# Performance work log

Measured on AMD Instinct MI355X. Metric: run time of the kernel, lower is better.

## Reference

```python
import jax, jax.numpy as jnp
import numpy as np

# FusionTransformer with input_resolution=(1, 8192): window_size collapses to 1,
# shift_size forced to 0, attn_mask is None. Inside WindowAttention each window
# has N=1 token, so the 512-truncation and the stride-2 subsample are no-ops,
# softmax over a single key yields 1, and the attention output equals v.
# We still compute q/k, the scaled logit, the relative-position bias (index
# table is [[0]]) and the softmax faithfully.

B, L, C = 8, 8192, 384
NH, CS = 8, 3
DIN = C // CS              # 128 = dim // channel_scale
HD = C // NH // CS         # 16  = per-head qk/v dim
SCALE = (C // NH) ** -0.5  # uses head_dim = dim // num_heads = 48 (as in source)
HID = int(DIN * 4.0)       # 512 mlp hidden
EPS = 1e-5                 # torch LayerNorm default


def setup_inputs() -> dict:
    key = jax.random.key(0)
    ks = jax.random.split(key, 8)
    w = lambda k, shape: jax.random.normal(k, shape, jnp.float32) * 0.02
    return {
        "x": jax.random.normal(ks[0], (B, L, C), jnp.float32),
        "g1": jnp.ones((C,), jnp.float32), "b1": jnp.zeros((C,), jnp.float32),
        "Wq": w(ks[1], (C, DIN)), "bq": jnp.zeros((DIN,), jnp.float32),
        "Wkv": w(ks[2], (C, 2 * DIN)), "bkv": jnp.zeros((2 * DIN,), jnp.float32),
        "rpb": w(ks[3], (1, NH)),  # (2*ws-1)^2 = 1 table rows at ws=1
        "Wp": w(ks[4], (DIN, DIN)), "bp": jnp.zeros((DIN,), jnp.float32),
        "g2": jnp.ones((DIN,), jnp.float32), "b2": jnp.zeros((DIN,), jnp.float32),
        "W1": w(ks[5], (DIN, HID)), "bm1": jnp.zeros((HID,), jnp.float32),
        "W2": w(ks[6], (HID, DIN)), "bm2": jnp.zeros((DIN,), jnp.float32),
    }


def _ln(x, g, b):
    m = x.mean(-1, keepdims=True)
    v = ((x - m) ** 2).mean(-1, keepdims=True)
    return (x - m) * jax.lax.rsqrt(v + EPS) * g + b


def reference(x, g1, b1, Wq, bq, Wkv, bkv, rpb, Wp, bp, g2, b2, W1, bm1, W2, bm2):
    Bx, Lx, _ = x.shape
    h = _ln(x, g1, b1)                       # norm1
    # window partition with ws=1: every token is a (N=1) window; B_ = B*L.
    q = h @ Wq + bq                          # (B, L, DIN)
    kv = h @ Wkv + bkv                       # (B, L, 2*DIN); split dim-0 of the
    k, v = kv[..., :DIN], kv[..., DIN:]      # reshape(...,2,NH,HD) -> k, v
    qh = q.reshape(Bx, Lx, NH, HD)
    kh = k.reshape(Bx, Lx, NH, HD)
    vh = v.reshape(Bx, Lx, NH, HD)
    # attn logits (B, L, NH, 1, 1) flattened: q*scale . k + rel-pos bias[idx=0]
    logits = jnp.einsum('blhd,blhd->blh', qh * SCALE, kh) + rpb[0]
    attn = jax.nn.softmax(logits[..., None], axis=-1)   # softmax over N=1 keys
    out = (attn * vh).reshape(Bx, Lx, NH * HD)          # attn @ v, heads merged
    y = out @ Wp + bp                                   # proj
    # residual branch: x = attn_out; x = x + mlp(norm2(x))
    z = y + (jax.nn.gelu(_ln(y, g2, b2) @ W1 + bm1, approximate=False) @ W2 + bm2)
    return z
```

## Files before the change

### kernel.cpp

```cpp
#include <hip/hip_runtime.h>
#include <hip/hip_bf16.h>
#include <stdint.h>


typedef __attribute__((ext_vector_type(8))) short bf16x8;
typedef __attribute__((ext_vector_type(4))) float f32x4;

__device__ __forceinline__ short f2bf(float f) {
  union { float f; unsigned u; } a; a.f = f;
  unsigned u = a.u;
  u += 0x7fffu + ((u >> 16) & 1u);
  return (short)(u >> 16);
}
__device__ __forceinline__ float bf2f(short s) {
  union { unsigned u; float f; } a; a.u = ((unsigned)(unsigned short)s) << 16;
  return a.f;
}
__device__ __forceinline__ float gelu_fast(float h) {
  float h2 = h * h;
  float w  = h * (2.3022082f + 0.1029471f * h2);
  float e  = __builtin_amdgcn_exp2f(w);
  float r  = __builtin_amdgcn_rcpf(e + 1.0f);
  return h - h * r;
}
__device__ __forceinline__ void gload_lds16(const void* g, void* l) {
  __builtin_amdgcn_global_load_lds(
      (const __attribute__((address_space(1))) unsigned*)g,
      (__attribute__((address_space(3))) unsigned*)l, 16, 0, 0);
}


__global__ void prep(const float* __restrict__ Wkv, const float* __restrict__ bkv,
                     const float* __restrict__ Wp,  const float* __restrict__ bp,
                     const float* __restrict__ W1,  const float* __restrict__ W2,
                     const float* __restrict__ g1,  const float* __restrict__ b1,
                     const float* __restrict__ g2,  const float* __restrict__ b2,
                     const float* __restrict__ bm1,
                     short* __restrict__ WcT, short* __restrict__ W1Ta,
                     short* __restrict__ W1Tb, short* __restrict__ W2Ta,
                     short* __restrict__ W2Tb, float* __restrict__ bc,
                     float* __restrict__ bm1c) {
  const int b = blockIdx.x, tid = threadIdx.x;
  if (b < 192) {
    __shared__ float wv[2][128];
    const int kk = tid >> 7, n = tid & 127, k = 2 * b + kk;
    wv[kk][n] = Wkv[k * 256 + 128 + n];
    __syncthreads();
    float s0 = 0, s1 = 0, s2 = 0, s3 = 0;
#pragma unroll 8
    for (int m = 0; m < 128; m += 4) {
      s0 += wv[kk][m]     * Wp[(m)     * 128 + n];
      s1 += wv[kk][m + 1] * Wp[(m + 1) * 128 + n];
      s2 += wv[kk][m + 2] * Wp[(m + 2) * 128 + n];
      s3 += wv[kk][m + 3] * Wp[(m + 3) * 128 + n];
    }
    WcT[n * 392 + k] = f2bf(g1[k] * (s0 + s1 + s2 + s3));
  } else if (b == 192) {
    __shared__ float t[128];
    if (tid < 128) {
      float a0 = 0, a1 = 0, a2 = 0, a3 = 0;
#pragma unroll 8
      for (int k = 0; k < 384; k += 4) {
        a0 += b1[k]     * Wkv[(k)     * 256 + 128 + tid];
        a1 += b1[k + 1] * Wkv[(k + 1) * 256 + 128 + tid];
        a2 += b1[k + 2] * Wkv[(k + 2) * 256 + 128 + tid];
        a3 += b1[k + 3] * Wkv[(k + 3) * 256 + 128 + tid];
      }
      t[tid] = a0 + a1 + a2 + a3 + bkv[128 + tid];
    }
    __syncthreads();
    if (tid < 128) {
      float s = bp[tid];
#pragma unroll 8
      for (int m = 0; m < 128; ++m) s += t[m] * Wp[m * 128 + tid];
      bc[tid] = s;
    }
  } else if (b < 449) {
    const int id = (b - 193) * 256 + tid;
    const int n = id & 511, k = id >> 9;
    const short v = f2bf(W1[k * 512 + n] * g2[k]);
    if (n < 256) W1Ta[n * 132 + k] = v;
    else         W1Tb[(n - 256) * 132 + k] = v;
  } else if (b < 705) {
    const int id = (b - 449) * 256 + tid;
    const int n = id & 127, k = id >> 7;
    const int ch = k >> 6, kk = k & 63;
    short* dst = (ch < 4) ? W2Ta : W2Tb;
    dst[((ch & 3) * 128 + n) * 68 + kk] = f2bf(W2[k * 128 + n]);
  } else {
    const int h = (b - 705) * 256 + tid;
    float s = bm1[h];
#pragma unroll 8
    for (int k = 0; k < 128; ++k) s += b2[k] * W1[k * 512 + h];
    bm1c[h] = s;
  }
}

__global__ __launch_bounds__(1024)
void k1(const float* __restrict__ x, const short* __restrict__ WcTg,
        const float* __restrict__ bcg,
        short* __restrict__ yb, short* __restrict__ lb) {
  __shared__ __align__(16) short WcT_l[128 * 392];
  __shared__ float bcf[128], css[128];
  const int tid = threadIdx.x, lane = tid & 63, w = tid >> 6;
  const int q = lane >> 4, c16 = lane & 15;

  for (int c = w; c < 98; c += 16)
    gload_lds16((const char*)WcTg + c * 1024 + lane * 16, (char*)WcT_l + c * 1024);
  if (tid < 32) ((float4*)bcf)[tid] = ((const float4*)bcg)[tid];
  __syncthreads();
  if (tid < 128) {
    float s0 = 0, s1 = 0, s2 = 0, s3 = 0;
    const short* row = WcT_l + tid * 392;
#pragma unroll 12
    for (int k = 0; k < 384; k += 4) {
      s0 += bf2f(row[k]); s1 += bf2f(row[k + 1]);
      s2 += bf2f(row[k + 2]); s3 += bf2f(row[k + 3]);
    }
    css[tid] = s0 + s1 + s2 + s3;
  }
  __syncthreads();

  const long band = (long)blockIdx.x * 16 + w;
  const float* xp = x + (band * 16 + c16) * 384 + q * 8;
  f32x4 yacc[8];
#pragma unroll
  for (int t = 0; t < 8; ++t) yacc[t] = (f32x4){0.f, 0.f, 0.f, 0.f};
  float s = 0.f, sq = 0.f;
#pragma unroll
  for (int ks = 0; ks < 12; ++ks) {
    const float4 va = *(const float4*)(xp + ks * 32);
    const float4 vb = *(const float4*)(xp + ks * 32 + 4);
    s  += va.x + va.y + va.z + va.w + vb.x + vb.y + vb.z + vb.w;
    sq += va.x * va.x + va.y * va.y + va.z * va.z + va.w * va.w
        + vb.x * vb.x + vb.y * vb.y + vb.z * vb.z + vb.w * vb.w;
    bf16x8 f;
    f[0] = f2bf(va.x); f[1] = f2bf(va.y); f[2] = f2bf(va.z); f[3] = f2bf(va.w);
    f[4] = f2bf(vb.x); f[5] = f2bf(vb.y); f[6] = f2bf(vb.z); f[7] = f2bf(vb.w);
#pragma unroll
    for (int t = 0; t < 8; ++t) {
      bf16x8 bfr = *(const bf16x8*)(WcT_l + (t * 16 + c16) * 392 + ks * 32 + q * 8);
      yacc[t] = __builtin_amdgcn_mfma_f32_16x16x32_bf16(f, bfr, yacc[t], 0, 0, 0);
    }
  }
  s  += __shfl_xor(s, 16);  s  += __shfl_xor(s, 32);
  sq += __shfl_xor(sq, 16); sq += __shfl_xor(sq, 32);
  const float mean = s * (1.f / 384.f);
  const float rs = rsqrtf(sq * (1.f / 384.f) - mean * mean + 1e-5f);
  float mr[4], rr[4];
#pragma unroll
  for (int r = 0; r < 4; ++r) {
    mr[r] = __shfl(mean, q * 4 + r);
    rr[r] = __shfl(rs,   q * 4 + r);
  }
  float sm[4] = {0, 0, 0, 0}, sv[4] = {0, 0, 0, 0};
#pragma unroll
  for (int t = 0; t < 8; ++t) {
    const float cst = css[t * 16 + c16];
    const float bct = bcf[t * 16 + c16];
#pragma unroll
    for (int r = 0; r < 4; ++r) {
      const float yv = rr[r] * (yacc[t][r] - mr[r] * cst) + bct;
      yacc[t][r] = yv; sm[r] += yv; sv[r] += yv * yv;
    }
  }
#pragma unroll
  for (int r = 0; r < 4; ++r) {
    sm[r] += __shfl_xor(sm[r], 1); sm[r] += __shfl_xor(sm[r], 2);
    sm[r] += __shfl_xor(sm[r], 4); sm[r] += __shfl_xor(sm[r], 8);
    sv[r] += __shfl_xor(sv[r], 1); sv[r] += __shfl_xor(sv[r], 2);
    sv[r] += __shfl_xor(sv[r], 4); sv[r] += __shfl_xor(sv[r], 8);
  }
  short* ybB = yb + band * 2048;
  short* lbB = lb + band * 2048;
#pragma unroll
  for (int r = 0; r < 4; ++r) {
    const float mn = sm[r] * (1.f / 128.f);
    const float rv = rsqrtf(sv[r] * (1.f / 128.f) - mn * mn + 1e-5f);
    bf16x8 yp;
#pragma unroll
    for (int t = 0; t < 8; ++t) {
      const float yv = yacc[t][r];
      yp[t] = f2bf(yv);
      lbB[((t * 4 + r) * 4 + q) * 16 + c16] = f2bf((yv - mn) * rv);
    }
    *(bf16x8*)(ybB + ((r * 4 + q) * 16 + c16) * 8) = yp;
  }
}

template <bool FINAL>
__global__ __launch_bounds__(1024)
void k2(const short* __restrict__ lb, short* __restrict__ ybuf,
        const short* __restrict__ W1Tg, const short* __restrict__ W2Tg,
        const float* __restrict__ bm1h, const float* __restrict__ bm2,
        float* __restrict__ out) {
  __shared__ __align__(16) short W1s[256 * 132];
  __shared__ __align__(16) short W2s[4 * 128 * 68];
  __shared__ __align__(16) short A3s[16][16 * 36];
  __shared__ float bm1s[256], bm2s[128];
  const int tid = threadIdx.x, lane = tid & 63, w = tid >> 6;
  const int q = lane >> 4, c16 = lane & 15;

  for (int c = w; c < 66; c += 16)
    gload_lds16((const char*)W1Tg + c * 1024 + lane * 16, (char*)W1s + c * 1024);
  for (int c = w; c < 68; c += 16)
    gload_lds16((const char*)W2Tg + c * 1024 + lane * 16, (char*)W2s + c * 1024);
  if (tid < 64) ((float4*)bm1s)[tid] = ((const float4*)bm1h)[tid];
  else if (tid < 96) ((float4*)bm2s)[tid - 64] = ((const float4*)bm2)[tid - 64];
  __syncthreads();

  const long band = (long)blockIdx.x * 16 + w;
  const short* lbB = lb + band * 2048;
  short* ybB = ybuf + band * 2048;
  bf16x8 a2f[4];
#pragma unroll
  for (int ks = 0; ks < 4; ++ks) {
    const int t = ks * 2 + (q >> 1);
    a2f[ks] = *(const bf16x8*)(lbB + ((t * 4 + (c16 & 3)) * 4 + (c16 >> 2)) * 16 + (q & 1) * 8);
  }
  f32x4 zacc[8];
#pragma unroll
  for (int t = 0; t < 8; ++t) zacc[t] = (f32x4){0.f, 0.f, 0.f, 0.f};
  short* a3 = A3s[w];

#pragma unroll
  for (int ch = 0; ch < 4; ++ch) {
#pragma unroll
    for (int sub = 0; sub < 2; ++sub) {
      f32x4 hacc[2];
      hacc[0] = (f32x4){0.f, 0.f, 0.f, 0.f};
      hacc[1] = (f32x4){0.f, 0.f, 0.f, 0.f};
#pragma unroll
      for (int ks = 0; ks < 4; ++ks)
#pragma unroll
        for (int tt = 0; tt < 2; ++tt) {
          bf16x8 bfr = *(const bf16x8*)(W1s + (ch * 64 + sub * 32 + tt * 16 + c16) * 132 + ks * 32 + q * 8);
          hacc[tt] = __builtin_amdgcn_mfma_f32_16x16x32_bf16(a2f[ks], bfr, hacc[tt], 0, 0, 0);
        }
#pragma unroll
      for (int tt = 0; tt < 2; ++tt) {
        const float bb = bm1s[ch * 64 + sub * 32 + tt * 16 + c16];
#pragma unroll
        for (int r = 0; r < 4; ++r) {
          const float h = hacc[tt][r] + bb;
          a3[(q * 4 + r) * 36 + tt * 16 + c16] = f2bf(gelu_fast(h));
        }
      }
      asm volatile("s_waitcnt lgkmcnt(0)" ::: "memory");
      bf16x8 af = *(const bf16x8*)(a3 + c16 * 36 + q * 8);
#pragma unroll
      for (int t = 0; t < 8; ++t) {
        bf16x8 bfr = *(const bf16x8*)(W2s + (ch * 128 + t * 16 + c16) * 68 + sub * 32 + q * 8);
        zacc[t] = __builtin_amdgcn_mfma_f32_16x16x32_bf16(af, bfr, zacc[t], 0, 0, 0);
      }
    }
  }
  bf16x8 yf[4];
#pragma unroll
  for (int r = 0; r < 4; ++r)
    yf[r] = *(const bf16x8*)(ybB + ((r * 4 + q) * 16 + c16) * 8);
  if (!FINAL) {
#pragma unroll
    for (int r = 0; r < 4; ++r) {
      bf16x8 zp;
#pragma unroll
      for (int t = 0; t < 8; ++t) zp[t] = f2bf(bf2f(yf[r][t]) + zacc[t][r]);
      *(bf16x8*)(ybB + ((r * 4 + q) * 16 + c16) * 8) = zp;
    }
  } else {
#pragma unroll
    for (int r = 0; r < 4; ++r) {
      const long rowg = band * 16 + q * 4 + r;
#pragma unroll
      for (int t = 0; t < 8; ++t)
        out[rowg * 128 + t * 16 + c16] = bf2f(yf[r][t]) + zacc[t][r] + bm2s[t * 16 + c16];
    }
  }
}

extern "C" void kernel_launch(void* const* d_in, const int* in_sizes, int n_in,
                              void* d_out, int out_size, void* d_ws, size_t ws_size,
                              hipStream_t stream) {
  const float* x   = (const float*)d_in[0];
  const float* g1  = (const float*)d_in[1];
  const float* b1  = (const float*)d_in[2];
  const float* Wkv = (const float*)d_in[5];
  const float* bkv = (const float*)d_in[6];
  const float* Wp  = (const float*)d_in[8];
  const float* bp  = (const float*)d_in[9];
  const float* g2  = (const float*)d_in[10];
  const float* b2  = (const float*)d_in[11];
  const float* W1  = (const float*)d_in[12];
  const float* bm1 = (const float*)d_in[13];
  const float* W2  = (const float*)d_in[14];
  const float* bm2 = (const float*)d_in[15];

  char* ws = (char*)d_ws;
  short* WcT  = (short*)(ws + 0);
  short* W1Ta = (short*)(ws + 100352);
  short* W2Ta = (short*)(ws + 167936);
  short* W1Tb = (short*)(ws + 237568);
  short* W2Tb = (short*)(ws + 305152);
  float* bc   = (float*)(ws + 374784);
  float* bm1c = (float*)(ws + 375296);
  short* ybuf = (short*)(ws + 378880);
  short* lb   = (short*)(ws + 17156096);

  prep<<<707, 256, 0, stream>>>(Wkv, bkv, Wp, bp, W1, W2, g1, b1, g2, b2, bm1,
                                WcT, W1Ta, W1Tb, W2Ta, W2Tb, bc, bm1c);
  k1<<<256, 1024, 0, stream>>>(x, WcT, bc, ybuf, lb);
  k2<false><<<256, 1024, 0, stream>>>(lb, ybuf, W1Ta, W2Ta, bm1c, bm2, (float*)d_out);
  k2<true><<<256, 1024, 0, stream>>>(lb, ybuf, W1Tb, W2Tb, bm1c + 256, bm2, (float*)d_out);
}
```

Before: 258.2 us.

## Fuse LN/projection and two MLP-half kernels into one kernel

Merges k1 and the two k2 launches into a single kernel. The kernel keeps y and the normalized activations in registers and reuses one shared-memory buffer, loading first the combined projection weights and then each MLP half's W1/W2 in turn. This removes the bf16 round trips through the ybuf/lb workspace and two kernel launches. In exchange, weight reloads now sit on each block's critical path behind barriers, and the large LDS footprint keeps occupancy at one block per CU.

New measurement: 335.5 us. 30.0% more time.

```diff
diff --git a/kernel.cpp b/kernel.cpp
--- a/kernel.cpp
+++ b/kernel.cpp
@@ -97,18 +97,25 @@
 }
 
 __global__ __launch_bounds__(1024)
-void k1(const float* __restrict__ x, const short* __restrict__ WcTg,
-        const float* __restrict__ bcg,
-        short* __restrict__ yb, short* __restrict__ lb) {
-  __shared__ __align__(16) short WcT_l[128 * 392];
-  __shared__ float bcf[128], css[128];
+void fused(const float* __restrict__ x, const short* __restrict__ WcTg,
+           const float* __restrict__ bcg,
+           const short* __restrict__ W1Tag, const short* __restrict__ W2Tag,
+           const short* __restrict__ W1Tbg, const short* __restrict__ W2Tbg,
+           const float* __restrict__ bm1c, const float* __restrict__ bm2,
+           float* __restrict__ out) {
+  __shared__ __align__(16) char Wbuf[137216];
+  __shared__ __align__(16) short A3s[16][576];
+  __shared__ float bcf[128], css[128], bm1s[512], bm2s[128];
   const int tid = threadIdx.x, lane = tid & 63, w = tid >> 6;
   const int q = lane >> 4, c16 = lane & 15;
 
   for (int c = w; c < 98; c += 16)
-    gload_lds16((const char*)WcTg + c * 1024 + lane * 16, (char*)WcT_l + c * 1024);
-  if (tid < 32) ((float4*)bcf)[tid] = ((const float4*)bcg)[tid];
+    gload_lds16((const char*)WcTg + c * 1024 + lane * 16, Wbuf + c * 1024);
+  if (tid < 128)      ((float4*)bm1s)[tid]       = ((const float4*)bm1c)[tid];
+  else if (tid < 160) ((float4*)bm2s)[tid - 128] = ((const float4*)bm2)[tid - 128];
+  else if (tid < 192) ((float4*)bcf)[tid - 160]  = ((const float4*)bcg)[tid - 160];
   __syncthreads();
+  const short* WcT_l = (const short*)Wbuf;
   if (tid < 128) {
     float s0 = 0, s1 = 0, s2 = 0, s3 = 0;
     const short* row = WcT_l + tid * 392;
@@ -153,6 +160,13 @@
     mr[r] = __shfl(mean, q * 4 + r);
     rr[r] = __shfl(rs,   q * 4 + r);
   }
+  __syncthreads();
+
+  for (int c = w; c < 66; c += 16)
+    gload_lds16((const char*)W1Tag + c * 1024 + lane * 16, Wbuf + c * 1024);
+  for (int c = w; c < 68; c += 16)
+    gload_lds16((const char*)W2Tag + c * 1024 + lane * 16, Wbuf + 67584 + c * 1024);
+
   float sm[4] = {0, 0, 0, 0}, sv[4] = {0, 0, 0, 0};
 #pragma unroll
   for (int t = 0; t < 8; ++t) {
@@ -171,110 +185,85 @@
     sv[r] += __shfl_xor(sv[r], 1); sv[r] += __shfl_xor(sv[r], 2);
     sv[r] += __shfl_xor(sv[r], 4); sv[r] += __shfl_xor(sv[r], 8);
   }
-  short* ybB = yb + band * 2048;
-  short* lbB = lb + band * 2048;
+  float mn[4], rv[4];
 #pragma unroll
   for (int r = 0; r < 4; ++r) {
-    const float mn = sm[r] * (1.f / 128.f);
-    const float rv = rsqrtf(sv[r] * (1.f / 128.f) - mn * mn + 1e-5f);
-    bf16x8 yp;
-#pragma unroll
-    for (int t = 0; t < 8; ++t) {
-      const float yv = yacc[t][r];
-      yp[t] = f2bf(yv);
-      lbB[((t * 4 + r) * 4 + q) * 16 + c16] = f2bf((yv - mn) * rv);
-    }
-    *(bf16x8*)(ybB + ((r * 4 + q) * 16 + c16) * 8) = yp;
-  }
-}
-
-template <bool FINAL>
-__global__ __launch_bounds__(1024)
-void k2(const short* __restrict__ lb, short* __restrict__ ybuf,
-        const short* __restrict__ W1Tg, const short* __restrict__ W2Tg,
-        const float* __restrict__ bm1h, const float* __restrict__ bm2,
-        float* __restrict__ out) {
-  __shared__ __align__(16) short W1s[256 * 132];
-  __shared__ __align__(16) short W2s[4 * 128 * 68];
-  __shared__ __align__(16) short A3s[16][16 * 36];
-  __shared__ float bm1s[256], bm2s[128];
-  const int tid = threadIdx.x, lane = tid & 63, w = tid >> 6;
-  const int q = lane >> 4, c16 = lane & 15;
-
-  for (int c = w; c < 66; c += 16)
-    gload_lds16((const char*)W1Tg + c * 1024 + lane * 16, (char*)W1s + c * 1024);
-  for (int c = w; c < 68; c += 16)
-    gload_lds16((const char*)W2Tg + c * 1024 + lane * 16, (char*)W2s + c * 1024);
-  if (tid < 64) ((float4*)bm1s)[tid] = ((const float4*)bm1h)[tid];
-  else if (tid < 96) ((float4*)bm2s)[tid - 64] = ((const float4*)bm2)[tid - 64];
-  __syncthreads();
-
-  const long band = (long)blockIdx.x * 16 + w;
-  const short* lbB = lb + band * 2048;
-  short* ybB = ybuf + band * 2048;
+    mn[r] = sm[r] * (1.f / 128.f);
+    rv[r] = rsqrtf(sv[r] * (1.f / 128.f) - mn[r] * mn[r] + 1e-5f);
+  }
+
+  short* A3w = A3s[w];
   bf16x8 a2f[4];
 #pragma unroll
   for (int ks = 0; ks < 4; ++ks) {
-    const int t = ks * 2 + (q >> 1);
-    a2f[ks] = *(const bf16x8*)(lbB + ((t * 4 + (c16 & 3)) * 4 + (c16 >> 2)) * 16 + (q & 1) * 8);
-  }
+#pragma unroll
+    for (int tt = 0; tt < 2; ++tt) {
+      const int t = ks * 2 + tt;
+#pragma unroll
+      for (int r = 0; r < 4; ++r)
+        A3w[tt * 256 + r * 64 + q * 16 + c16] = f2bf((yacc[t][r] - mn[r]) * rv[r]);
+    }
+    asm volatile("s_waitcnt lgkmcnt(0)" ::: "memory");
+    a2f[ks] = *(const bf16x8*)(A3w + (q >> 1) * 256 + (c16 & 3) * 64 +
+                               (c16 >> 2) * 16 + (q & 1) * 8);
+  }
+
   f32x4 zacc[8];
 #pragma unroll
   for (int t = 0; t < 8; ++t) zacc[t] = (f32x4){0.f, 0.f, 0.f, 0.f};
-  short* a3 = A3s[w];
-
-#pragma unroll
-  for (int ch = 0; ch < 4; ++ch) {
-#pragma unroll
-    for (int sub = 0; sub < 2; ++sub) {
-      f32x4 hacc[2];
-      hacc[0] = (f32x4){0.f, 0.f, 0.f, 0.f};
-      hacc[1] = (f32x4){0.f, 0.f, 0.f, 0.f};
-#pragma unroll
-      for (int ks = 0; ks < 4; ++ks)
+  const short* W1s = (const short*)Wbuf;
+  const short* W2s = (const short*)(Wbuf + 67584);
+
+  for (int half = 0; half < 2; ++half) {
+    if (half) {
+      __syncthreads();
+      for (int c = w; c < 66; c += 16)
+        gload_lds16((const char*)W1Tbg + c * 1024 + lane * 16, Wbuf + c * 1024);
+      for (int c = w; c < 68; c += 16)
+        gload_lds16((const char*)W2Tbg + c * 1024 + lane * 16, Wbuf + 67584 + c * 1024);
+    }
+    __syncthreads();
+
+#pragma unroll
+    for (int ch = 0; ch < 4; ++ch) {
+#pragma unroll
+      for (int sub = 0; sub < 2; ++sub) {
+        f32x4 hacc[2];
+        hacc[0] = (f32x4){0.f, 0.f, 0.f, 0.f};
+        hacc[1] = (f32x4){0.f, 0.f, 0.f, 0.f};
+#pragma unroll
+        for (int ks = 0; ks < 4; ++ks)
+#pragma unroll
+          for (int tt = 0; tt < 2; ++tt) {
+            bf16x8 bfr = *(const bf16x8*)(W1s + (ch * 64 + sub * 32 + tt * 16 + c16) * 132 + ks * 32 + q * 8);
+            hacc[tt] = __builtin_amdgcn_mfma_f32_16x16x32_bf16(a2f[ks], bfr, hacc[tt], 0, 0, 0);
+          }
 #pragma unroll
         for (int tt = 0; tt < 2; ++tt) {
-          bf16x8 bfr = *(const bf16x8*)(W1s + (ch * 64 + sub * 32 + tt * 16 + c16) * 132 + ks * 32 + q * 8);
-          hacc[tt] = __builtin_amdgcn_mfma_f32_16x16x32_bf16(a2f[ks], bfr, hacc[tt], 0, 0, 0);
+          const float bb = bm1s[half * 256 + ch * 64 + sub * 32 + tt * 16 + c16];
+#pragma unroll
+          for (int r = 0; r < 4; ++r) {
+            const float h = hacc[tt][r] + bb;
+            A3w[(q * 4 + r) * 36 + tt * 16 + c16] = f2bf(gelu_fast(h));
+          }
         }
-#pragma unroll
-      for (int tt = 0; tt < 2; ++tt) {
-        const float bb = bm1s[ch * 64 + sub * 32 + tt * 16 + c16];
-#pragma unroll
-        for (int r = 0; r < 4; ++r) {
-          const float h = hacc[tt][r] + bb;
-          a3[(q * 4 + r) * 36 + tt * 16 + c16] = f2bf(gelu_fast(h));
+        asm volatile("s_waitcnt lgkmcnt(0)" ::: "memory");
+        bf16x8 af = *(const bf16x8*)(A3w + c16 * 36 + q * 8);
+#pragma unroll
+        for (int t = 0; t < 8; ++t) {
+          bf16x8 bfr = *(const bf16x8*)(W2s + (ch * 128 + t * 16 + c16) * 68 + sub * 32 + q * 8);
+          zacc[t] = __builtin_amdgcn_mfma_f32_16x16x32_bf16(af, bfr, zacc[t], 0, 0, 0);
         }
       }
-      asm volatile("s_waitcnt lgkmcnt(0)" ::: "memory");
-      bf16x8 af = *(const bf16x8*)(a3 + c16 * 36 + q * 8);
-#pragma unroll
-      for (int t = 0; t < 8; ++t) {
-        bf16x8 bfr = *(const bf16x8*)(W2s + (ch * 128 + t * 16 + c16) * 68 + sub * 32 + q * 8);
-        zacc[t] = __builtin_amdgcn_mfma_f32_16x16x32_bf16(af, bfr, zacc[t], 0, 0, 0);
-      }
-    }
-  }
-  bf16x8 yf[4];
-#pragma unroll
-  for (int r = 0; r < 4; ++r)
-    yf[r] = *(const bf16x8*)(ybB + ((r * 4 + q) * 16 + c16) * 8);
-  if (!FINAL) {
-#pragma unroll
-    for (int r = 0; r < 4; ++r) {
-      bf16x8 zp;
-#pragma unroll
-      for (int t = 0; t < 8; ++t) zp[t] = f2bf(bf2f(yf[r][t]) + zacc[t][r]);
-      *(bf16x8*)(ybB + ((r * 4 + q) * 16 + c16) * 8) = zp;
-    }
-  } else {
-#pragma unroll
-    for (int r = 0; r < 4; ++r) {
-      const long rowg = band * 16 + q * 4 + r;
-#pragma unroll
-      for (int t = 0; t < 8; ++t)
-        out[rowg * 128 + t * 16 + c16] = bf2f(yf[r][t]) + zacc[t][r] + bm2s[t * 16 + c16];
-    }
+    }
+  }
+
+#pragma unroll
+  for (int r = 0; r < 4; ++r) {
+    const long rowg = band * 16 + q * 4 + r;
+#pragma unroll
+    for (int t = 0; t < 8; ++t)
+      out[rowg * 128 + t * 16 + c16] = yacc[t][r] + zacc[t][r] + bm2s[t * 16 + c16];
   }
 }
 
@@ -303,12 +292,9 @@
   short* W2Tb = (short*)(ws + 305152);
   float* bc   = (float*)(ws + 374784);
   float* bm1c = (float*)(ws + 375296);
-  short* ybuf = (short*)(ws + 378880);
-  short* lb   = (short*)(ws + 17156096);
 
   prep<<<707, 256, 0, stream>>>(Wkv, bkv, Wp, bp, W1, W2, g1, b1, g2, b2, bm1,
                                 WcT, W1Ta, W1Tb, W2Ta, W2Tb, bc, bm1c);
-  k1<<<256, 1024, 0, stream>>>(x, WcT, bc, ybuf, lb);
-  k2<false><<<256, 1024, 0, stream>>>(lb, ybuf, W1Ta, W2Ta, bm1c, bm2, (float*)d_out);
-  k2<true><<<256, 1024, 0, stream>>>(lb, ybuf, W1Tb, W2Tb, bm1c + 256, bm2, (float*)d_out);
-}
+  fused<<<256, 1024, 0, stream>>>(x, WcT, bc, W1Ta, W2Ta, W1Tb, W2Tb,
+                                  bm1c, bm2, (float*)d_out);
+}
```
